# Kernel tuning notes

Measured on AMD Instinct MI355X. Metric: run time of the kernel, lower is better.

The kernel has to match this reference:

```python
import jax, jax.numpy as jnp
import numpy as np

EMBED_DIM = 1024
NUM_HEADS = 16
HEAD_DIM = EMBED_DIM // NUM_HEADS


def setup_inputs() -> dict:
    key = jax.random.key(0)
    ks = jax.random.split(key, 6)
    s = 1.0 / np.sqrt(EMBED_DIM)
    x = jax.random.normal(ks[0], (2, 2048, EMBED_DIM), dtype=jnp.float32)
    Wk = jax.random.uniform(ks[1], (EMBED_DIM, EMBED_DIM), jnp.float32, -s, s)
    Wq = jax.random.uniform(ks[2], (EMBED_DIM, EMBED_DIM), jnp.float32, -s, s)
    Wv = jax.random.uniform(ks[3], (EMBED_DIM, EMBED_DIM), jnp.float32, -s, s)
    Wo = jax.random.uniform(ks[4], (EMBED_DIM, EMBED_DIM), jnp.float32, -s, s)
    bo = jax.random.uniform(ks[5], (EMBED_DIM,), jnp.float32, -s, s)
    return {"x": x, "Wq": Wq, "Wk": Wk, "Wv": Wv, "Wo": Wo, "bo": bo}


def reference(x, Wq, Wk, Wv, Wo, bo):
    b, s, e = x.shape
    h, d = NUM_HEADS, HEAD_DIM
    scale = d ** (-0.5)
    # nn.Linear: y = x @ W.T ; here W stored as [out, in] -> use W.T
    q = (x @ Wq.T).reshape(b, s, h, d).transpose(0, 2, 1, 3)  # b h s d
    k = (x @ Wk.T).reshape(b, s, h, d).transpose(0, 2, 1, 3)
    v = (x @ Wv.T).reshape(b, s, h, d).transpose(0, 2, 1, 3)
    logits = jnp.einsum('bhqd,bhkd->bhqk', q, k) * scale
    attn = jax.nn.softmax(logits, axis=-1)
    out = jnp.einsum('bhqk,bhkd->bhqd', attn, v)
    out = out.transpose(0, 2, 1, 3).reshape(b, s, e)
    return out @ Wo.T + bo
```

## Files before the change

### kernel.cpp

```cpp
#include <hip/hip_runtime.h>
#include <hip/hip_bf16.h>

using short8 = __attribute__((ext_vector_type(8))) short;
using f32x4  = __attribute__((ext_vector_type(4))) float;
using uint4v = __attribute__((ext_vector_type(4))) unsigned;

#if __has_builtin(__builtin_amdgcn_exp2f)
#define EXP2(x) __builtin_amdgcn_exp2f(x)
#else
#define EXP2(x) exp2f(x)
#endif

__device__ __forceinline__ short f2bf(float f) {
    union { float f; unsigned u; } v; v.f = f;
    unsigned r = v.u + 0x7fffu + ((v.u >> 16) & 1u);
    return (short)(r >> 16);
}
__device__ __forceinline__ unsigned pack_trunc(float a, float b) {
    union { float f; unsigned u; } ua, ub; ua.f = a; ub.f = b;
#if __has_builtin(__builtin_amdgcn_perm)
    return __builtin_amdgcn_perm(ub.u, ua.u, 0x07060302u);
#else
    return (ub.u & 0xFFFF0000u) | (ua.u >> 16);
#endif
}
__device__ __forceinline__ void async_copy16(const short* g, short* s) {
    __builtin_amdgcn_global_load_lds(
        (const __attribute__((address_space(1))) void*)g,
        (__attribute__((address_space(3))) void*)s, 16, 0, 0);
}

__global__ __launch_bounds__(256) void cvt_f32_bf16(
    const float* __restrict__ s0, const float* __restrict__ s1,
    const float* __restrict__ s2, const float* __restrict__ s3,
    const float* __restrict__ s4,
    short* __restrict__ d0, short* __restrict__ d1, short* __restrict__ d2,
    short* __restrict__ d3, short* __restrict__ d4) {
    const int bid = blockIdx.x;
    const float* s; short* d; int base;
    if (bid < 4096) {
        s = s0; d = d0; base = bid << 10;
    } else {
        const int r = bid - 4096;
        base = (r & 1023) << 10;
        switch (r >> 10) {
            case 0: s = s1; d = d1; break;
            case 1: s = s2; d = d2; break;
            case 2: s = s3; d = d3; break;
            default: s = s4; d = d4; break;
        }
    }
    const int idx = base + threadIdx.x * 4;
    float4 v = *(const float4*)(s + idx);
    short4 o;
    o.x = f2bf(v.x); o.y = f2bf(v.y); o.z = f2bf(v.z); o.w = f2bf(v.w);
    *(short4*)(d + idx) = o;
}

template <int MODE>
__device__ __forceinline__ void gemm_body(const short* __restrict__ A,
                                          const short* __restrict__ B,
                                          short* __restrict__ C,
                                          float scale,
                                          short* __restrict__ As,
                                          short* __restrict__ Bs) {
    constexpr int Kd = 1024, Nd = 1024, Sd = 2048;

    const int tid  = threadIdx.x;
    const int w    = tid >> 6, lane = tid & 63;
    const int quad = lane >> 4, l16 = lane & 15;
    const int xr   = l16 & 7;
    const int wm   = (w >> 1) * 64, wn = (w & 1) * 64;
    const int bm   = blockIdx.y * 128, bn = blockIdx.x * 128;

    f32x4 acc[4][4];
#pragma unroll
    for (int i = 0; i < 4; ++i)
#pragma unroll
        for (int j = 0; j < 4; ++j) acc[i][j] = (f32x4){0.f, 0.f, 0.f, 0.f};

    for (int k0 = 0; k0 < Kd; k0 += 64) {
        __syncthreads();
#pragma unroll
        for (int c = 0; c < 4; ++c) {
            int li   = c * 256 + tid;
            int row  = li >> 3;
            int gcol = ((li & 7) ^ (row & 7)) * 8;
            async_copy16(A + (size_t)(bm + row) * Kd + k0 + gcol, &As[li * 8]);
            async_copy16(B + (size_t)(bn + row) * Kd + k0 + gcol, &Bs[li * 8]);
        }
        __syncthreads();

#pragma unroll
        for (int kk = 0; kk < 2; ++kk) {
            short8 af[4], bfv[4];
#pragma unroll
            for (int mi = 0; mi < 4; ++mi) {
                const int r = wm + mi * 16 + l16;
                af[mi] = *(const short8*)(
                    &As[r * 64 + (((kk * 4 + quad) ^ xr) * 8)]);
            }
#pragma unroll
            for (int ni = 0; ni < 4; ++ni) {
                const int r = wn + ni * 16 + l16;
                bfv[ni] = *(const short8*)(
                    &Bs[r * 64 + (((kk * 4 + quad) ^ xr) * 8)]);
            }
#pragma unroll
            for (int mi = 0; mi < 4; ++mi)
#pragma unroll
                for (int ni = 0; ni < 4; ++ni) {
                    if constexpr (MODE == 2)
                        acc[mi][ni] = __builtin_amdgcn_mfma_f32_16x16x32_bf16(
                            bfv[ni], af[mi], acc[mi][ni], 0, 0, 0);
                    else
                        acc[mi][ni] = __builtin_amdgcn_mfma_f32_16x16x32_bf16(
                            af[mi], bfv[ni], acc[mi][ni], 0, 0, 0);
                }
        }
    }

    if constexpr (MODE == 2) {
#pragma unroll
        for (int mi = 0; mi < 4; ++mi) {
            const int m_g = bm + wm + mi * 16 + l16;
            const int b_  = m_g >> 11, s_ = m_g & 2047;
#pragma unroll
            for (int ni = 0; ni < 4; ++ni)
#pragma unroll
                for (int r = 0; r < 4; ++r) {
                    const int n_g = bn + wn + ni * 16 + quad * 4 + r;
                    C[(size_t)b_ * Nd * Sd + (size_t)n_g * Sd + s_] =
                        f2bf(acc[mi][ni][r]);
                }
        }
    } else {
#pragma unroll
        for (int ni = 0; ni < 4; ++ni) {
            const int colg = bn + wn + ni * 16 + l16;
#pragma unroll
            for (int mi = 0; mi < 4; ++mi)
#pragma unroll
                for (int r = 0; r < 4; ++r) {
                    const int rowg = bm + wm + mi * 16 + quad * 4 + r;
                    C[(size_t)rowg * Nd + colg] = f2bf(acc[mi][ni][r] * scale);
                }
        }
    }
}

#define CSC 0.18033688f

__global__ __launch_bounds__(256, 3) void proj_gemm(
    const short* __restrict__ X,
    const short* __restrict__ Wq, const short* __restrict__ Wk,
    const short* __restrict__ Wv,
    short* __restrict__ Qo, short* __restrict__ Ko, short* __restrict__ VTo) {
    __shared__ __align__(16) short As[128 * 64];
    __shared__ __align__(16) short Bs[128 * 64];
    if (blockIdx.z == 0)
        gemm_body<0>(X, Wq, Qo, CSC, As, Bs);
    else if (blockIdx.z == 1)
        gemm_body<0>(X, Wk, Ko, 1.0f, As, Bs);
    else
        gemm_body<2>(X, Wv, VTo, 1.0f, As, Bs);
}

__global__ __launch_bounds__(256, 2) void out_gemm(
    const short* __restrict__ A, const short* __restrict__ B,
    const float* __restrict__ bias, float* __restrict__ C) {
    constexpr int Kd = 1024, Nd = 1024;
    __shared__ __align__(16) short As[64 * 64];
    __shared__ __align__(16) short Bs[128 * 64];

    const int tid  = threadIdx.x;
    const int w    = tid >> 6, lane = tid & 63;
    const int quad = lane >> 4, l16 = lane & 15;
    const int xr   = l16 & 7;
    const int wm   = (w >> 1) * 32, wn = (w & 1) * 64;
    const int bm   = blockIdx.y * 64, bn = blockIdx.x * 128;

    f32x4 acc[2][4];
#pragma unroll
    for (int i = 0; i < 2; ++i)
#pragma unroll
        for (int j = 0; j < 4; ++j) acc[i][j] = (f32x4){0.f, 0.f, 0.f, 0.f};

    for (int k0 = 0; k0 < Kd; k0 += 64) {
        __syncthreads();
#pragma unroll
        for (int c = 0; c < 2; ++c) {
            int li   = c * 256 + tid;
            int row  = li >> 3;
            int gcol = ((li & 7) ^ (row & 7)) * 8;
            async_copy16(A + (size_t)(bm + row) * Kd + k0 + gcol, &As[li * 8]);
        }
#pragma unroll
        for (int c = 0; c < 4; ++c) {
            int li   = c * 256 + tid;
            int row  = li >> 3;
            int gcol = ((li & 7) ^ (row & 7)) * 8;
            async_copy16(B + (size_t)(bn + row) * Kd + k0 + gcol, &Bs[li * 8]);
        }
        __syncthreads();

#pragma unroll
        for (int kk = 0; kk < 2; ++kk) {
            short8 af[2], bfv[4];
#pragma unroll
            for (int mi = 0; mi < 2; ++mi) {
                const int r = wm + mi * 16 + l16;
                af[mi] = *(const short8*)(
                    &As[r * 64 + (((kk * 4 + quad) ^ xr) * 8)]);
            }
#pragma unroll
            for (int ni = 0; ni < 4; ++ni) {
                const int r = wn + ni * 16 + l16;
                bfv[ni] = *(const short8*)(
                    &Bs[r * 64 + (((kk * 4 + quad) ^ xr) * 8)]);
            }
#pragma unroll
            for (int mi = 0; mi < 2; ++mi)
#pragma unroll
                for (int ni = 0; ni < 4; ++ni)
                    acc[mi][ni] = __builtin_amdgcn_mfma_f32_16x16x32_bf16(
                        af[mi], bfv[ni], acc[mi][ni], 0, 0, 0);
        }
    }

#pragma unroll
    for (int ni = 0; ni < 4; ++ni) {
        const int colg = bn + wn + ni * 16 + l16;
        const float bv = bias[colg];
#pragma unroll
        for (int mi = 0; mi < 2; ++mi)
#pragma unroll
            for (int r = 0; r < 4; ++r) {
                const int rowg = bm + wm + mi * 16 + quad * 4 + r;
                C[(size_t)rowg * Nd + colg] = acc[mi][ni][r] + bv;
            }
    }
}

__global__ __launch_bounds__(256, 2) void attn_kernel(
    const short* __restrict__ Q, const short* __restrict__ K,
    const short* __restrict__ VT, short* __restrict__ O) {
    constexpr int S = 2048, E = 1024, NT = S / 64;
    __shared__ __align__(16) short Ks[2][64 * 64];
    __shared__ __align__(16) short Vs[3][64 * 64];

    const int tid  = threadIdx.x;
    const int w    = tid >> 6, lane = tid & 63;
    const int quad = lane >> 4, l16 = lane & 15;

    const int bid  = blockIdx.x;
    const int xcd  = bid & 7, slot = bid >> 3;
    const int qt   = slot & 15;
    const int bh   = xcd + ((slot >> 4) << 3);
    const int b    = bh >> 4, h = bh & 15;

    const int    q0   = qt * 128 + w * 32;
    const size_t base = (size_t)b * S * E;
    const size_t vtb  = (size_t)b * E * S;
    const int    hc   = h * 64;
    const int    xr   = l16 & 7;

    short8 aq[2][2];
#pragma unroll
    for (int qg = 0; qg < 2; ++qg) {
        const short* qp = Q + base + (size_t)(q0 + qg * 16 + l16) * E + hc + quad * 8;
        aq[qg][0] = *(const short8*)(qp);
        aq[qg][1] = *(const short8*)(qp + 32);
    }

    f32x4 oT[2][4], o_sum[2];
#pragma unroll
    for (int qg = 0; qg < 2; ++qg) {
        o_sum[qg] = (f32x4){0.f, 0.f, 0.f, 0.f};
#pragma unroll
        for (int i = 0; i < 4; ++i) oT[qg][i] = (f32x4){0.f, 0.f, 0.f, 0.f};
    }

    int          kdst[2], vdst0[2], vdst1[2];
    const short* kga[2];
    const short* vga[2];
#pragma unroll
    for (int c = 0; c < 2; ++c) {
        int li = c * 256 + tid, row = li >> 3, cc = li & 7;
        kdst[c] = row * 64 + ((cc ^ (row & 7)) * 8);
        int c0   = 4 * (cc >> 2) + 2 * (cc & 1);
        int boff = 4 * ((cc >> 1) & 1);
        vdst0[c] = row * 64 + ((c0 ^ (row & 7)) * 8) + boff;
        vdst1[c] = row * 64 + (((c0 + 1) ^ (row & 7)) * 8) + boff;
        kga[c]   = K + base + (size_t)row * E + hc + cc * 8;
        vga[c]   = VT + vtb + (size_t)(hc + row) * S + cc * 8;
    }

    short8 kr[2], vr[2];
    auto load_regs = [&](int t) {
#pragma unroll
        for (int c = 0; c < 2; ++c) {
            kr[c] = *(const short8*)(kga[c] + (size_t)t * 64 * E);
            vr[c] = *(const short8*)(vga[c] + t * 64);
        }
    };
    auto store_regs = [&](short* Kn, short* Vn) {
#pragma unroll
        for (int c = 0; c < 2; ++c) {
            *(short8*)(&Kn[kdst[c]]) = kr[c];
            short4 lo, hi;
            lo.x = kr[c][0];
            lo.x = vr[c][0]; lo.y = vr[c][1]; lo.z = vr[c][2]; lo.w = vr[c][3];
            hi.x = vr[c][4]; hi.y = vr[c][5]; hi.z = vr[c][6]; hi.w = vr[c][7];
            *(short4*)(&Vn[vdst0[c]]) = lo;
            *(short4*)(&Vn[vdst1[c]]) = hi;
        }
    };

    const short8 ones = (short8){0x3F80, 0x3F80, 0x3F80, 0x3F80,
                                 0x3F80, 0x3F80, 0x3F80, 0x3F80};
    const float  LB   = 0.00281502f;

    uint4v pkvA[2][2], pkvB[2][2];

    auto qk_half = [&](const short* Kc, uint4v (&pc)[2][2], int h) {
#pragma unroll
        for (int kh = 0; kh < 2; ++kh) {
            const int    kn  = h * 2 + kh;
            const short* kb  = &Kc[(kn * 16 + l16) * 64];
            short8       bk0 = *(const short8*)(kb + ((quad ^ xr) * 8));
            short8       bk1 = *(const short8*)(kb + (((quad + 4) ^ xr) * 8));
#pragma unroll
            for (int qg = 0; qg < 2; ++qg) {
                f32x4 a = (f32x4){LB, LB, LB, LB};
                a = __builtin_amdgcn_mfma_f32_16x16x32_bf16(bk0, aq[qg][0], a, 0, 0, 0);
                a = __builtin_amdgcn_mfma_f32_16x16x32_bf16(bk1, aq[qg][1], a, 0, 0, 0);
                pc[qg][h][kh * 2]     = pack_trunc(EXP2(a[0]), EXP2(a[1]));
                pc[qg][h][kh * 2 + 1] = pack_trunc(EXP2(a[2]), EXP2(a[3]));
            }
        }
    };
    auto pv_half = [&](const short* Vp, uint4v (&pp)[2][2], int ks) {
        short8 pf[2];
#pragma unroll
        for (int qg = 0; qg < 2; ++qg) {
            union { uint4v u; short8 s; } cv;
            cv.u   = pp[qg][ks];
            pf[qg] = cv.s;
            o_sum[qg] = __builtin_amdgcn_mfma_f32_16x16x32_bf16(
                ones, pf[qg], o_sum[qg], 0, 0, 0);
        }
#pragma unroll
        for (int ni = 0; ni < 4; ++ni) {
            const int rv = ni * 16 + l16;
            short8 vb =
                *(const short8*)(&Vp[rv * 64 + (((ks * 4 + quad) ^ xr) * 8)]);
#pragma unroll
            for (int qg = 0; qg < 2; ++qg)
                oT[qg][ni] = __builtin_amdgcn_mfma_f32_16x16x32_bf16(
                    vb, pf[qg], oT[qg][ni], 0, 0, 0);
        }
    };

    auto body = [&](int kt, uint4v (&pp)[2][2], uint4v (&pc)[2][2]) {
        if (kt + 1 < NT) {
            store_regs(Ks[(kt + 1) & 1], Vs[(kt + 1) % 3]);
            if (kt + 2 < NT) load_regs(kt + 2);
        }
        const short* Kc = Ks[kt & 1];
        const short* Vp = Vs[(kt - 1) % 3];
        __builtin_amdgcn_s_setprio(1);
        pv_half(Vp, pp, 0);
        qk_half(Kc, pc, 0);
        pv_half(Vp, pp, 1);
        qk_half(Kc, pc, 1);
        __builtin_amdgcn_s_setprio(0);
        __syncthreads();
    };

    load_regs(0);
    store_regs(Ks[0], Vs[0]);
    load_regs(1);
    __syncthreads();
    store_regs(Ks[1], Vs[1]);
    load_regs(2);
    __builtin_amdgcn_s_setprio(1);
    qk_half(Ks[0], pkvA, 0);
    qk_half(Ks[0], pkvA, 1);
    __builtin_amdgcn_s_setprio(0);
    __syncthreads();

#pragma unroll 1
    for (int kt = 1; kt < NT - 1; kt += 2) {
        body(kt, pkvA, pkvB);
        body(kt + 1, pkvB, pkvA);
    }
    body(NT - 1, pkvA, pkvB);
    __builtin_amdgcn_s_setprio(1);
    pv_half(Vs[(NT - 1) % 3], pkvB, 0);
    pv_half(Vs[(NT - 1) % 3], pkvB, 1);
    __builtin_amdgcn_s_setprio(0);

#pragma unroll
    for (int qg = 0; qg < 2; ++qg) {
        const float inv = 1.0f / o_sum[qg][0];
        const int   qg_ = q0 + qg * 16 + l16;
#pragma unroll
        for (int ni = 0; ni < 4; ++ni) {
            short4 ov;
            ov.x = f2bf(oT[qg][ni][0] * inv);
            ov.y = f2bf(oT[qg][ni][1] * inv);
            ov.z = f2bf(oT[qg][ni][2] * inv);
            ov.w = f2bf(oT[qg][ni][3] * inv);
            *(short4*)(&O[base + (size_t)qg_ * E + hc + ni * 16 + quad * 4]) = ov;
        }
    }
}

extern "C" void kernel_launch(void* const* d_in, const int* in_sizes, int n_in,
                              void* d_out, int out_size, void* d_ws, size_t ws_size,
                              hipStream_t stream) {
    const float* x  = (const float*)d_in[0];
    const float* Wq = (const float*)d_in[1];
    const float* Wk = (const float*)d_in[2];
    const float* Wv = (const float*)d_in[3];
    const float* Wo = (const float*)d_in[4];
    const float* bo = (const float*)d_in[5];
    float* out = (float*)d_out;

    constexpr int XN = 2 * 2048 * 1024;
    constexpr int WN = 1024 * 1024;

    short* Xb  = (short*)d_ws;
    short* Wqb = Xb + XN;
    short* Wkb = Wqb + WN;
    short* Wvb = Wkb + WN;
    short* Wob = Wvb + WN;
    short* Qb  = Wob + WN;
    short* Kb  = Qb + XN;
    short* VTb = Kb + XN;

    cvt_f32_bf16<<<dim3(8192), 256, 0, stream>>>(
        x, Wq, Wk, Wv, Wo, Xb, Wqb, Wkb, Wvb, Wob);
    proj_gemm<<<dim3(8, 32, 3), 256, 0, stream>>>(Xb, Wqb, Wkb, Wvb, Qb, Kb, VTb);
    attn_kernel<<<dim3(512), 256, 0, stream>>>(Qb, Kb, VTb, Xb );
    out_gemm<<<dim3(8, 64), 256, 0, stream>>>(Xb, Wob, bo, out);
}
```

Measured before the change: 167.0 us.

## Load V fragments directly from global into registers, dropping V shared-memory staging

Stops staging V tiles through a triple-buffered shared-memory array. Each wave now loads its own V MFMA fragments straight from global memory into double-buffered registers, one tile ahead. This removes the LDS writes and reads for V and cuts LDS footprint, which may allow more occupancy. In exchange, each of the four waves redundantly fetches the same V tile with narrow 8-byte global loads, and register pressure rises under the 2-blocks-per-SM launch bound.

```diff
diff --git a/kernel.cpp b/kernel.cpp
--- a/kernel.cpp
+++ b/kernel.cpp
@@ -247,7 +247,6 @@
     const short* __restrict__ VT, short* __restrict__ O) {
     constexpr int S = 2048, E = 1024, NT = S / 64;
     __shared__ __align__(16) short Ks[2][64 * 64];
-    __shared__ __align__(16) short Vs[3][64 * 64];
 
     const int tid  = threadIdx.x;
     const int w    = tid >> 6, lane = tid & 63;
@@ -281,40 +280,40 @@
         for (int i = 0; i < 4; ++i) oT[qg][i] = (f32x4){0.f, 0.f, 0.f, 0.f};
     }
 
-    int          kdst[2], vdst0[2], vdst1[2];
+    int          kdst[2];
     const short* kga[2];
-    const short* vga[2];
 #pragma unroll
     for (int c = 0; c < 2; ++c) {
         int li = c * 256 + tid, row = li >> 3, cc = li & 7;
         kdst[c] = row * 64 + ((cc ^ (row & 7)) * 8);
-        int c0   = 4 * (cc >> 2) + 2 * (cc & 1);
-        int boff = 4 * ((cc >> 1) & 1);
-        vdst0[c] = row * 64 + ((c0 ^ (row & 7)) * 8) + boff;
-        vdst1[c] = row * 64 + (((c0 + 1) ^ (row & 7)) * 8) + boff;
-        kga[c]   = K + base + (size_t)row * E + hc + cc * 8;
-        vga[c]   = VT + vtb + (size_t)(hc + row) * S + cc * 8;
-    }
-
-    short8 kr[2], vr[2];
-    auto load_regs = [&](int t) {
-#pragma unroll
-        for (int c = 0; c < 2; ++c) {
+        kga[c]  = K + base + (size_t)row * E + hc + cc * 8;
+    }
+
+    short8 kr[2];
+    auto load_k = [&](int t) {
+#pragma unroll
+        for (int c = 0; c < 2; ++c)
             kr[c] = *(const short8*)(kga[c] + (size_t)t * 64 * E);
-            vr[c] = *(const short8*)(vga[c] + t * 64);
-        }
-    };
-    auto store_regs = [&](short* Kn, short* Vn) {
-#pragma unroll
-        for (int c = 0; c < 2; ++c) {
+    };
+    auto store_k = [&](short* Kn) {
+#pragma unroll
+        for (int c = 0; c < 2; ++c)
             *(short8*)(&Kn[kdst[c]]) = kr[c];
-            short4 lo, hi;
-            lo.x = kr[c][0];
-            lo.x = vr[c][0]; lo.y = vr[c][1]; lo.z = vr[c][2]; lo.w = vr[c][3];
-            hi.x = vr[c][4]; hi.y = vr[c][5]; hi.z = vr[c][6]; hi.w = vr[c][7];
-            *(short4*)(&Vn[vdst0[c]]) = lo;
-            *(short4*)(&Vn[vdst1[c]]) = hi;
-        }
+    };
+
+    const short* vbase = VT + vtb + (size_t)(hc + l16) * S + 4 * quad;
+    short8 vfA[2][4], vfB[2][4];
+    auto load_vf = [&](short8 (&vf)[2][4], int t) {
+#pragma unroll
+        for (int ks = 0; ks < 2; ++ks)
+#pragma unroll
+            for (int ni = 0; ni < 4; ++ni) {
+                const short* p = vbase + (size_t)(ni * 16) * S + t * 64 + 32 * ks;
+                short4 lo = *(const short4*)(p);
+                short4 hi = *(const short4*)(p + 16);
+                vf[ks][ni] = (short8){lo.x, lo.y, lo.z, lo.w,
+                                      hi.x, hi.y, hi.z, hi.w};
+            }
     };
 
     const short8 ones = (short8){0x3F80, 0x3F80, 0x3F80, 0x3F80,
@@ -340,7 +339,7 @@
             }
         }
     };
-    auto pv_half = [&](const short* Vp, uint4v (&pp)[2][2], int ks) {
+    auto pv_half = [&](short8 (&vf)[2][4], uint4v (&pp)[2][2], int ks) {
         short8 pf[2];
 #pragma unroll
         for (int qg = 0; qg < 2; ++qg) {
@@ -352,38 +351,37 @@
         }
 #pragma unroll
         for (int ni = 0; ni < 4; ++ni) {
-            const int rv = ni * 16 + l16;
-            short8 vb =
-                *(const short8*)(&Vp[rv * 64 + (((ks * 4 + quad) ^ xr) * 8)]);
 #pragma unroll
             for (int qg = 0; qg < 2; ++qg)
                 oT[qg][ni] = __builtin_amdgcn_mfma_f32_16x16x32_bf16(
-                    vb, pf[qg], oT[qg][ni], 0, 0, 0);
-        }
-    };
-
-    auto body = [&](int kt, uint4v (&pp)[2][2], uint4v (&pc)[2][2]) {
+                    vf[ks][ni], pf[qg], oT[qg][ni], 0, 0, 0);
+        }
+    };
+
+    auto body = [&](int kt, uint4v (&pp)[2][2], uint4v (&pc)[2][2],
+                    short8 (&vprev)[2][4], short8 (&vcur)[2][4]) {
+        load_vf(vcur, kt);
         if (kt + 1 < NT) {
-            store_regs(Ks[(kt + 1) & 1], Vs[(kt + 1) % 3]);
-            if (kt + 2 < NT) load_regs(kt + 2);
+            store_k(Ks[(kt + 1) & 1]);
+            if (kt + 2 < NT) load_k(kt + 2);
         }
         const short* Kc = Ks[kt & 1];
-        const short* Vp = Vs[(kt - 1) % 3];
         __builtin_amdgcn_s_setprio(1);
-        pv_half(Vp, pp, 0);
+        pv_half(vprev, pp, 0);
         qk_half(Kc, pc, 0);
-        pv_half(Vp, pp, 1);
+        pv_half(vprev, pp, 1);
         qk_half(Kc, pc, 1);
         __builtin_amdgcn_s_setprio(0);
         __syncthreads();
     };
 
-    load_regs(0);
-    store_regs(Ks[0], Vs[0]);
-    load_regs(1);
+    load_k(0);
+    store_k(Ks[0]);
+    load_k(1);
     __syncthreads();
-    store_regs(Ks[1], Vs[1]);
-    load_regs(2);
+    load_vf(vfA, 0);
+    store_k(Ks[1]);
+    load_k(2);
     __builtin_amdgcn_s_setprio(1);
     qk_half(Ks[0], pkvA, 0);
     qk_half(Ks[0], pkvA, 1);
@@ -392,13 +390,13 @@
 
 #pragma unroll 1
     for (int kt = 1; kt < NT - 1; kt += 2) {
-        body(kt, pkvA, pkvB);
-        body(kt + 1, pkvB, pkvA);
-    }
-    body(NT - 1, pkvA, pkvB);
+        body(kt, pkvA, pkvB, vfA, vfB);
+        body(kt + 1, pkvB, pkvA, vfB, vfA);
+    }
+    body(NT - 1, pkvA, pkvB, vfA, vfB);
     __builtin_amdgcn_s_setprio(1);
-    pv_half(Vs[(NT - 1) % 3], pkvB, 0);
-    pv_half(Vs[(NT - 1) % 3], pkvB, 1);
+    pv_half(vfB, pkvB, 0);
+    pv_half(vfB, pkvB, 1);
     __builtin_amdgcn_s_setprio(0);
 
 #pragma unroll
```

Result: slower. 253.0 us (+51.5%).
